# Optimization experiments

Hardware: AMD Instinct MI355X
Metric: run time of the kernel (lower is better)

Reference implementation:

```python
import jax, jax.numpy as jnp
import numpy as np

B, N, E = 256, 4096, 65536  # graphs, nodes/graph (64*64), edges/graph


def setup_inputs() -> dict:
    key = jax.random.key(0)
    k = jax.random.split(key, 6)
    x = jax.random.normal(k[0], (B, N, 3), dtype=jnp.float32)
    src = jax.random.randint(k[1], (E,), 0, N, dtype=jnp.int32)
    dst = jax.random.randint(k[2], (E,), 0, N, dtype=jnp.int32)
    W1 = jax.random.normal(k[3], (3, 64), dtype=jnp.float32) * 0.3
    b1 = jnp.zeros((64,), dtype=jnp.float32)
    Wfc = jax.random.normal(k[4], (N * 64, 1), dtype=jnp.float32) * 0.002
    bfc = jnp.zeros((1,), dtype=jnp.float32)
    return {"x": x, "W1": W1, "b1": b1, "Wfc": Wfc, "bfc": bfc,
            "src": src, "dst": dst}


def reference(x, W1, b1, Wfc, bfc, src, dst):
    # DGL GraphConv, norm='both': h = relu(D_in^{-1/2} A D_out^{-1/2} x W + b)
    ones = jnp.ones((E,), dtype=x.dtype)
    deg_out = jax.ops.segment_sum(ones, src, num_segments=N)
    deg_in = jax.ops.segment_sum(ones, dst, num_segments=N)
    c_src = jax.lax.rsqrt(jnp.maximum(deg_out, 1.0))  # [N]
    c_dst = jax.lax.rsqrt(jnp.maximum(deg_in, 1.0))   # [N]
    # gather normalized source features, scatter-add into destinations
    msg = (x * c_src[None, :, None])[:, src]          # [B, E, 3]
    agg = jnp.zeros_like(x).at[:, dst].add(msg)       # [B, N, 3]
    h = jax.nn.relu((agg * c_dst[None, :, None]) @ W1 + b1)  # [B, N, 64]
    # fc: flatten per graph, Linear(N*64 -> 1) + sigmoid
    logits = h.reshape(x.shape[0], -1) @ Wfc + bfc    # [B, 1]
    return jax.nn.sigmoid(logits)
```

## Files before the change

### kernel.cpp

```cpp
#include <hip/hip_runtime.h>
#include <math.h>

#define Bg 256
#define Nn 4096
#define Ee 65536
#define Kk (Nn * 3)

__global__ __launch_bounds__(256) void k_degrees(const int* __restrict__ src,
                                                 const int* __restrict__ dst,
                                                 int* __restrict__ deg_out,
                                                 int* __restrict__ deg_in) {
    int e = blockIdx.x * 256 + threadIdx.x;
    if (e < Ee) {
        atomicAdd(&deg_out[src[e]], 1);
        atomicAdd(&deg_in[dst[e]], 1);
    }
}

__global__ __launch_bounds__(256) void k_norm_scan(const int* __restrict__ deg_out,
                                                   const int* __restrict__ deg_in,
                                                   float* __restrict__ c_src,
                                                   float* __restrict__ c_dst,
                                                   int* __restrict__ row_ptr) {
    int t = threadIdx.x;
    int base = t * 16;
    int local[16];
    int s = 0;
#pragma unroll
    for (int i = 0; i < 16; i++) {
        int di = deg_in[base + i];
        local[i] = di;
        s += di;
        c_dst[base + i] = rsqrtf(fmaxf((float)di, 1.0f));
        int dq = deg_out[base + i];
        c_src[base + i] = rsqrtf(fmaxf((float)dq, 1.0f));
    }
    int lane = t & 63, w = t >> 6;
    int inc = s;
#pragma unroll
    for (int d = 1; d < 64; d <<= 1) {
        int v = __shfl_up(inc, d, 64);
        if (lane >= d) inc += v;
    }
    __shared__ int wtot[4], woff[4];
    if (lane == 63) wtot[w] = inc;
    __syncthreads();
    if (t == 0) { int run = 0; for (int i = 0; i < 4; i++) { woff[i] = run; run += wtot[i]; } }
    __syncthreads();
    int run = inc - s + woff[w];
#pragma unroll
    for (int i = 0; i < 16; i++) { row_ptr[base + i] = run; run += local[i]; }
    if (t == 255) row_ptr[Nn] = run;
}

__global__ __launch_bounds__(256) void k_fill(const int* __restrict__ src,
                                              const int* __restrict__ dst,
                                              const int* __restrict__ row_ptr,
                                              int* __restrict__ cursor,
                                              int* __restrict__ csr_src) {
    int e = blockIdx.x * 256 + threadIdx.x;
    if (e < Ee) {
        int d = dst[e];
        int ofs = atomicAdd(&cursor[d], 1);
        csr_src[row_ptr[d] + ofs] = src[e];
    }
}

__global__ __launch_bounds__(256) void k_transpose(const float* __restrict__ x,
                                                   const float* __restrict__ c_src,
                                                   float* __restrict__ xs2) {
    __shared__ float tile[64][193];
    int t = threadIdx.x;
    int n0 = blockIdx.x * 64;
    int bq = blockIdx.y;
    const float* xb = x + (size_t)bq * 64 * Kk + (size_t)n0 * 3;
#pragma unroll 8
    for (int i = 0; i < 48; i++) {
        int flat = i * 256 + t;
        int bi = flat / 192, kk = flat - bi * 192;
        tile[bi][kk] = xb[(size_t)bi * Kk + kk];
    }
    __syncthreads();
    float* outp = xs2 + (size_t)bq * (Nn * 192) + (size_t)n0 * 192;
#pragma unroll 8
    for (int i = 0; i < 48; i++) {
        int o = i * 256 + t;
        int nn = o / 192; int r = o - nn * 192;
        int bl = r / 3;   int c = r - bl * 3;
        outp[o] = tile[bl][nn * 3 + c] * c_src[n0 + nn];
    }
}

template <int NPB>
__global__ __launch_bounds__(64) void k_main(const float* __restrict__ xs2,
                                             const float* __restrict__ W1,
                                             const float* __restrict__ b1,
                                             const float* __restrict__ Wfc,
                                             const float* __restrict__ c_dst,
                                             const int* __restrict__ row_ptr,
                                             const int* __restrict__ csr_src,
                                             float* __restrict__ partial) {
    __shared__ float4 sW14[64];
    __shared__ float sWfc[NPB * 64];
    int t = threadIdx.x;
    int bq = blockIdx.x & 3;
    int g  = blockIdx.x >> 2;
    int n0 = g * NPB;
    sW14[t] = make_float4(W1[t], W1[64 + t], W1[128 + t], b1[t]);
#pragma unroll
    for (int j = 0; j < NPB; j++) sWfc[j * 64 + t] = Wfc[(n0 + j) * 64 + t];
    __syncthreads();

    const float* slab = xs2 + (size_t)bq * (Nn * 192);
    float acc[NPB][3];
#pragma unroll
    for (int j = 0; j < NPB; j++) {
        int s0 = row_ptr[n0 + j], s1 = row_ptr[n0 + j + 1];
        float a0 = 0.f, a1 = 0.f, a2 = 0.f;
        int i = s0;
        for (; i + 4 <= s1; i += 4) {
            const float* p0 = slab + csr_src[i]     * 192 + t * 3;
            const float* p1 = slab + csr_src[i + 1] * 192 + t * 3;
            const float* p2 = slab + csr_src[i + 2] * 192 + t * 3;
            const float* p3 = slab + csr_src[i + 3] * 192 + t * 3;
            float u0 = p0[0], u1 = p0[1], u2 = p0[2];
            float v0 = p1[0], v1 = p1[1], v2 = p1[2];
            float w0 = p2[0], w1 = p2[1], w2 = p2[2];
            float z0 = p3[0], z1 = p3[1], z2 = p3[2];
            a0 += (u0 + v0) + (w0 + z0);
            a1 += (u1 + v1) + (w1 + z1);
            a2 += (u2 + v2) + (w2 + z2);
        }
        for (; i < s1; i++) {
            const float* p = slab + csr_src[i] * 192 + t * 3;
            a0 += p[0]; a1 += p[1]; a2 += p[2];
        }
        float cd = c_dst[n0 + j];
        acc[j][0] = a0 * cd; acc[j][1] = a1 * cd; acc[j][2] = a2 * cd;
    }

    float part[NPB];
#pragma unroll
    for (int j = 0; j < NPB; j++) part[j] = 0.f;
#pragma unroll 16
    for (int f = 0; f < 64; f++) {
        float4 w = sW14[f];
#pragma unroll
        for (int j = 0; j < NPB; j++) {
            float h = fmaf(acc[j][0], w.x, fmaf(acc[j][1], w.y, fmaf(acc[j][2], w.z, w.w)));
            h = fmaxf(h, 0.f);
            part[j] = fmaf(h, sWfc[j * 64 + f], part[j]);
        }
    }
    float tot = 0.f;
#pragma unroll
    for (int j = 0; j < NPB; j++) tot += part[j];
    partial[(size_t)g * 256 + bq * 64 + t] = tot;
}

__global__ __launch_bounds__(256) void k_reduce(const float* __restrict__ partial,
                                                float* __restrict__ out_acc,
                                                int chunk) {
    int t = threadIdx.x;
    int g0 = blockIdx.x * chunk;
    float s = 0.f;
    for (int g = 0; g < chunk; g++) s += partial[(size_t)(g0 + g) * 256 + t];
    atomicAdd(&out_acc[t], s);
}

__global__ __launch_bounds__(256) void k_final(const float* __restrict__ out_acc,
                                               const float* __restrict__ bfc,
                                               float* __restrict__ out) {
    int t = threadIdx.x;
    float v = out_acc[t] + bfc[0];
    out[t] = 1.0f / (1.0f + expf(-v));
}

extern "C" void kernel_launch(void* const* d_in, const int* in_sizes, int n_in,
                              void* d_out, int out_size, void* d_ws, size_t ws_size,
                              hipStream_t stream) {
    const float* x   = (const float*)d_in[0];
    const float* W1  = (const float*)d_in[1];
    const float* b1  = (const float*)d_in[2];
    const float* Wfc = (const float*)d_in[3];
    const float* bfc = (const float*)d_in[4];
    const int*   src = (const int*)d_in[5];
    const int*   dst = (const int*)d_in[6];
    float* out = (float*)d_out;

    char* ws = (char*)d_ws;
    float* xs2 = (float*)ws;
    const size_t Z = (size_t)Kk * Bg * 4;
    int*   deg_out = (int*)(ws + Z);
    int*   deg_in  = (int*)(ws + Z + 16384);
    int*   cursor  = (int*)(ws + Z + 32768);
    float* out_acc = (float*)(ws + Z + 49152);
    float* c_src   = (float*)(ws + Z + 50176);
    float* c_dst   = (float*)(ws + Z + 66560);
    int*   row_ptr = (int*)(ws + Z + 82944);
    int*   csr_src = (int*)(ws + Z + 99344);
    size_t poff    = Z + 99344 + 262144;
    float* partial = (float*)(ws + poff);

    hipMemsetAsync(ws + Z, 0, 50176, stream);
    k_degrees<<<Ee / 256, 256, 0, stream>>>(src, dst, deg_out, deg_in);
    k_norm_scan<<<1, 256, 0, stream>>>(deg_out, deg_in, c_src, c_dst, row_ptr);
    k_fill<<<Ee / 256, 256, 0, stream>>>(src, dst, row_ptr, cursor, csr_src);
    k_transpose<<<dim3(Nn / 64, 4), 256, 0, stream>>>(x, c_src, xs2);

    if (ws_size >= poff + (size_t)(Nn / 2) * 256 * 4) {
        const int NPB = 2;
        k_main<NPB><<<(Nn / NPB) * 4, 64, 0, stream>>>(xs2, W1, b1, Wfc, c_dst, row_ptr, csr_src, partial);
        k_reduce<<<256, 256, 0, stream>>>(partial, out_acc, (Nn / NPB) / 256);
    } else {
        const int NPB = 8;
        k_main<NPB><<<(Nn / NPB) * 4, 64, 0, stream>>>(xs2, W1, b1, Wfc, c_dst, row_ptr, csr_src, partial);
        k_reduce<<<256, 256, 0, stream>>>(partial, out_acc, (Nn / NPB) / 256);
    }
    k_final<<<1, 256, 0, stream>>>(out_acc, bfc, out);
}
```

Baseline: 130.1 us.

## Vectorize transpose with float4 and give each wavefront its own node in k_main

The transpose kernel now loads and stores float4 vectors through a padded float4 shared tile instead of scalar floats. This cuts the number of memory instructions. k_main changes from 64-thread blocks that walk NPB nodes one after another to 256-thread blocks where each of the four wavefronts gathers one destination node. The per-wavefront partials are reduced in shared memory, with a launch-bounds occupancy hint. The partial buffer shrinks, so k_reduce runs with fewer blocks, and the workspace-size fallback path is removed. This exposes more parallel gather latency hiding, at the cost of an extra sync and shared reduction per block.

```diff
diff --git a/kernel.cpp b/kernel.cpp
--- a/kernel.cpp
+++ b/kernel.cpp
@@ -69,93 +69,102 @@
 __global__ __launch_bounds__(256) void k_transpose(const float* __restrict__ x,
                                                    const float* __restrict__ c_src,
                                                    float* __restrict__ xs2) {
-    __shared__ float tile[64][193];
+    __shared__ float4 tile4[64][49];
     int t = threadIdx.x;
     int n0 = blockIdx.x * 64;
     int bq = blockIdx.y;
     const float* xb = x + (size_t)bq * 64 * Kk + (size_t)n0 * 3;
-#pragma unroll 8
-    for (int i = 0; i < 48; i++) {
-        int flat = i * 256 + t;
-        int bi = flat / 192, kk = flat - bi * 192;
-        tile[bi][kk] = xb[(size_t)bi * Kk + kk];
-    }
-    __syncthreads();
-    float* outp = xs2 + (size_t)bq * (Nn * 192) + (size_t)n0 * 192;
-#pragma unroll 8
-    for (int i = 0; i < 48; i++) {
-        int o = i * 256 + t;
-        int nn = o / 192; int r = o - nn * 192;
-        int bl = r / 3;   int c = r - bl * 3;
-        outp[o] = tile[bl][nn * 3 + c] * c_src[n0 + nn];
-    }
-}
-
-template <int NPB>
-__global__ __launch_bounds__(64) void k_main(const float* __restrict__ xs2,
-                                             const float* __restrict__ W1,
-                                             const float* __restrict__ b1,
-                                             const float* __restrict__ Wfc,
-                                             const float* __restrict__ c_dst,
-                                             const int* __restrict__ row_ptr,
-                                             const int* __restrict__ csr_src,
-                                             float* __restrict__ partial) {
+#pragma unroll
+    for (int i = 0; i < 12; i++) {
+        int idx = i * 256 + t;
+        int bi = idx / 48, j = idx - bi * 48;
+        tile4[bi][j] = ((const float4*)(xb + (size_t)bi * Kk))[j];
+    }
+    __syncthreads();
+    const float* tile = (const float*)tile4;
+    float4* outp = (float4*)(xs2 + (size_t)bq * (Nn * 192) + (size_t)n0 * 192);
+#pragma unroll
+    for (int i = 0; i < 12; i++) {
+        int o4 = i * 256 + t;
+        int nn = o4 / 48, q = o4 - nn * 48;
+        int f0 = q * 4;
+        float cs = c_src[n0 + nn];
+        float4 v;
+        {
+            int f = f0;     int bl = f / 3, c = f - 3 * bl; v.x = tile[bl * 196 + nn * 3 + c];
+        }
+        {
+            int f = f0 + 1; int bl = f / 3, c = f - 3 * bl; v.y = tile[bl * 196 + nn * 3 + c];
+        }
+        {
+            int f = f0 + 2; int bl = f / 3, c = f - 3 * bl; v.z = tile[bl * 196 + nn * 3 + c];
+        }
+        {
+            int f = f0 + 3; int bl = f / 3, c = f - 3 * bl; v.w = tile[bl * 196 + nn * 3 + c];
+        }
+        v.x *= cs; v.y *= cs; v.z *= cs; v.w *= cs;
+        outp[o4] = v;
+    }
+}
+
+__global__ __launch_bounds__(256, 6) void k_main(const float* __restrict__ xs2,
+                                                 const float* __restrict__ W1,
+                                                 const float* __restrict__ b1,
+                                                 const float* __restrict__ Wfc,
+                                                 const float* __restrict__ c_dst,
+                                                 const int* __restrict__ row_ptr,
+                                                 const int* __restrict__ csr_src,
+                                                 float* __restrict__ partial) {
     __shared__ float4 sW14[64];
-    __shared__ float sWfc[NPB * 64];
-    int t = threadIdx.x;
+    __shared__ float sWfc[4][64];
+    __shared__ float red[4][64];
+    int t = threadIdx.x & 63;
+    int w = threadIdx.x >> 6;
     int bq = blockIdx.x & 3;
     int g  = blockIdx.x >> 2;
-    int n0 = g * NPB;
-    sW14[t] = make_float4(W1[t], W1[64 + t], W1[128 + t], b1[t]);
-#pragma unroll
-    for (int j = 0; j < NPB; j++) sWfc[j * 64 + t] = Wfc[(n0 + j) * 64 + t];
+    int n  = g * 4 + w;
+    if (w == 0) sW14[t] = make_float4(W1[t], W1[64 + t], W1[128 + t], b1[t]);
+    sWfc[w][t] = Wfc[n * 64 + t];
     __syncthreads();
 
     const float* slab = xs2 + (size_t)bq * (Nn * 192);
-    float acc[NPB][3];
-#pragma unroll
-    for (int j = 0; j < NPB; j++) {
-        int s0 = row_ptr[n0 + j], s1 = row_ptr[n0 + j + 1];
-        float a0 = 0.f, a1 = 0.f, a2 = 0.f;
-        int i = s0;
-        for (; i + 4 <= s1; i += 4) {
-            const float* p0 = slab + csr_src[i]     * 192 + t * 3;
-            const float* p1 = slab + csr_src[i + 1] * 192 + t * 3;
-            const float* p2 = slab + csr_src[i + 2] * 192 + t * 3;
-            const float* p3 = slab + csr_src[i + 3] * 192 + t * 3;
-            float u0 = p0[0], u1 = p0[1], u2 = p0[2];
-            float v0 = p1[0], v1 = p1[1], v2 = p1[2];
-            float w0 = p2[0], w1 = p2[1], w2 = p2[2];
-            float z0 = p3[0], z1 = p3[1], z2 = p3[2];
-            a0 += (u0 + v0) + (w0 + z0);
-            a1 += (u1 + v1) + (w1 + z1);
-            a2 += (u2 + v2) + (w2 + z2);
-        }
-        for (; i < s1; i++) {
-            const float* p = slab + csr_src[i] * 192 + t * 3;
-            a0 += p[0]; a1 += p[1]; a2 += p[2];
-        }
-        float cd = c_dst[n0 + j];
-        acc[j][0] = a0 * cd; acc[j][1] = a1 * cd; acc[j][2] = a2 * cd;
-    }
-
-    float part[NPB];
-#pragma unroll
-    for (int j = 0; j < NPB; j++) part[j] = 0.f;
-#pragma unroll 16
+    int s0 = row_ptr[n], s1 = row_ptr[n + 1];
+    int vt = t * 3;
+    float a0 = 0.f, a1 = 0.f, a2 = 0.f;
+    int i = s0;
+    for (; i + 4 <= s1; i += 4) {
+        const float* p0 = slab + csr_src[i]     * 192 + vt;
+        const float* p1 = slab + csr_src[i + 1] * 192 + vt;
+        const float* p2 = slab + csr_src[i + 2] * 192 + vt;
+        const float* p3 = slab + csr_src[i + 3] * 192 + vt;
+        float u0 = p0[0], u1 = p0[1], u2 = p0[2];
+        float v0 = p1[0], v1 = p1[1], v2 = p1[2];
+        float w0 = p2[0], w1 = p2[1], w2 = p2[2];
+        float z0 = p3[0], z1 = p3[1], z2 = p3[2];
+        a0 += (u0 + v0) + (w0 + z0);
+        a1 += (u1 + v1) + (w1 + z1);
+        a2 += (u2 + v2) + (w2 + z2);
+    }
+    for (; i < s1; i++) {
+        const float* p = slab + csr_src[i] * 192 + vt;
+        a0 += p[0]; a1 += p[1]; a2 += p[2];
+    }
+    float cd = c_dst[n];
+    a0 *= cd; a1 *= cd; a2 *= cd;
+
+    float part = 0.f;
+#pragma unroll 8
     for (int f = 0; f < 64; f++) {
-        float4 w = sW14[f];
-#pragma unroll
-        for (int j = 0; j < NPB; j++) {
-            float h = fmaf(acc[j][0], w.x, fmaf(acc[j][1], w.y, fmaf(acc[j][2], w.z, w.w)));
-            h = fmaxf(h, 0.f);
-            part[j] = fmaf(h, sWfc[j * 64 + f], part[j]);
-        }
-    }
-    float tot = 0.f;
-#pragma unroll
-    for (int j = 0; j < NPB; j++) tot += part[j];
-    partial[(size_t)g * 256 + bq * 64 + t] = tot;
+        float4 wv = sW14[f];
+        float h = fmaf(a0, wv.x, fmaf(a1, wv.y, fmaf(a2, wv.z, wv.w)));
+        part = fmaf(fmaxf(h, 0.f), sWfc[w][f], part);
+    }
+    red[w][t] = part;
+    __syncthreads();
+    if (w == 0) {
+        float tot = (red[0][t] + red[1][t]) + (red[2][t] + red[3][t]);
+        partial[(size_t)g * 256 + bq * 64 + t] = tot;
+    }
 }
 
 __global__ __launch_bounds__(256) void k_reduce(const float* __restrict__ partial,
@@ -199,23 +208,14 @@
     float* c_dst   = (float*)(ws + Z + 66560);
     int*   row_ptr = (int*)(ws + Z + 82944);
     int*   csr_src = (int*)(ws + Z + 99344);
-    size_t poff    = Z + 99344 + 262144;
-    float* partial = (float*)(ws + poff);
+    float* partial = (float*)(ws + Z + 361488);
 
     hipMemsetAsync(ws + Z, 0, 50176, stream);
     k_degrees<<<Ee / 256, 256, 0, stream>>>(src, dst, deg_out, deg_in);
     k_norm_scan<<<1, 256, 0, stream>>>(deg_out, deg_in, c_src, c_dst, row_ptr);
     k_fill<<<Ee / 256, 256, 0, stream>>>(src, dst, row_ptr, cursor, csr_src);
     k_transpose<<<dim3(Nn / 64, 4), 256, 0, stream>>>(x, c_src, xs2);
-
-    if (ws_size >= poff + (size_t)(Nn / 2) * 256 * 4) {
-        const int NPB = 2;
-        k_main<NPB><<<(Nn / NPB) * 4, 64, 0, stream>>>(xs2, W1, b1, Wfc, c_dst, row_ptr, csr_src, partial);
-        k_reduce<<<256, 256, 0, stream>>>(partial, out_acc, (Nn / NPB) / 256);
-    } else {
-        const int NPB = 8;
-        k_main<NPB><<<(Nn / NPB) * 4, 64, 0, stream>>>(xs2, W1, b1, Wfc, c_dst, row_ptr, csr_src, partial);
-        k_reduce<<<256, 256, 0, stream>>>(partial, out_acc, (Nn / NPB) / 256);
-    }
+    k_main<<<1024 * 4, 256, 0, stream>>>(xs2, W1, b1, Wfc, c_dst, row_ptr, csr_src, partial);
+    k_reduce<<<64, 256, 0, stream>>>(partial, out_acc, 16);
     k_final<<<1, 256, 0, stream>>>(out_acc, bfc, out);
 }
```

Measured after the change: 126.0 us. 1.03x faster.
